# Kernel optimization log

Hardware: AMD Instinct MI355X
Metric: run time of the kernel (lower is better)

Reference implementation:

```python
import jax, jax.numpy as jnp
import numpy as np

N_NODES = 100000
N_EDGES = 1600000
D_IN = 128
D_OUT = 128


def setup_inputs() -> dict:
    key = jax.random.key(0)
    k1, k2, k3, k4 = jax.random.split(key, 4)
    feat = jax.random.normal(k1, (N_NODES, D_IN), dtype=jnp.float32)
    weight = jax.random.normal(k2, (D_IN, D_OUT), dtype=jnp.float32) * (1.0 / np.sqrt(D_IN))
    src = jax.random.randint(k3, (N_EDGES,), 0, N_NODES, dtype=jnp.int64)
    dst = jax.random.randint(k4, (N_EDGES,), 0, N_NODES, dtype=jnp.int64)
    return {"feat": feat, "weight": weight, "src": src, "dst": dst}


def reference(feat, weight, src, dst):
    n = feat.shape[0]
    ones = jnp.ones(src.shape[0], dtype=feat.dtype)
    # norm == 'both': scale source features by out_degree^{-1/2}
    out_deg = jnp.clip(jax.ops.segment_sum(ones, src, num_segments=n), 1.0)
    feat_src = feat * (out_deg ** -0.5)[:, None]  # [N, D_in]
    # update_all(copy_src, sum): gather src features, segment-sum into dst
    agg = jax.ops.segment_sum(feat_src[src], dst, num_segments=n)  # [N, D_in]
    # dense transform with external weight
    rst = agg @ weight  # [N, D_out]
    # destination-side normalization by in_degree^{-1/2}
    in_deg = jnp.clip(jax.ops.segment_sum(ones, dst, num_segments=n), 1.0)
    rst = rst * (in_deg ** -0.5)[:, None]
    return rst
```

## Files before the change

kernel.cpp:

```cpp
#include <hip/hip_runtime.h>
#include <stdint.h>


#define DIM 128
#define BK 64
#define MAXB 2048
#define CAPB 1280
#define SK 128
#define MAXS 1024
#define CAPS 2560
#define PT 512
#define EPT 13
#define CHUNK (PT * EPT)

typedef unsigned int uint;
typedef unsigned short ushortT;
typedef __attribute__((ext_vector_type(8))) _Float16 f16x8;
typedef __attribute__((ext_vector_type(4))) float f32x4;

__device__ __forceinline__ ushortT f2bf(float x) {
    uint u = __float_as_uint(x);
    u = (u + 0x7FFFu + ((u >> 16) & 1u)) >> 16;
    return (ushortT)u;
}
__device__ __forceinline__ float bflo(uint u) { return __uint_as_float(u << 16); }
__device__ __forceinline__ float bfhi(uint u) { return __uint_as_float(u & 0xffff0000u); }

union H16 { _Float16 h; ushortT u; };
__device__ __forceinline__ ushortT f2h_bits(float x) {
    H16 t; t.h = (_Float16)x; return t.u;
}

__global__ __launch_bounds__(PT) void part(
    const int* __restrict__ src, const int* __restrict__ dst,
    int* __restrict__ curB, int* __restrict__ curS,
    int* __restrict__ pairs, unsigned char* __restrict__ srcb,
    int E, int NPB, int NPS) {
    __shared__ int cD[MAXB], lofD[MAXB];
    __shared__ int cS[MAXS], lofS[MAXS];
    __shared__ int bufD[CHUNK];
    __shared__ ushortT bufB[CHUNK];
    __shared__ unsigned char bufS[CHUNK];
    __shared__ int wtotD[8], wtotS[8];

    int tid = threadIdx.x;
    long long base = (long long)blockIdx.x * CHUNK;
    for (int i = tid; i < MAXB; i += PT) cD[i] = 0;
    for (int i = tid; i < MAXS; i += PT) cS[i] = 0;
    __syncthreads();

    int sv[EPT], dv[EPT], lrD[EPT], lrS[EPT];
#pragma unroll
    for (int j = 0; j < EPT; ++j) {
        long long e = base + tid + j * PT;
        bool ok = e < E;
        int s = 0, d = 0;
        if (ok) { s = src[e]; d = dst[e]; }
        sv[j] = s; dv[j] = d;
        lrD[j] = ok ? atomicAdd(&cD[d >> 6], 1) : 0;
        lrS[j] = ok ? atomicAdd(&cS[s >> 7], 1) : 0;
    }
    __syncthreads();

    {
        int lane = tid & 63, wv = tid >> 6;
        int b0 = tid << 2;
        int s0 = cD[b0], s1 = cD[b0 + 1], s2 = cD[b0 + 2], s3 = cD[b0 + 3];
        int tsum = s0 + s1 + s2 + s3;
        int incl = tsum;
        for (int o = 1; o < 64; o <<= 1) {
            int y = __shfl_up(incl, o, 64);
            if (lane >= o) incl += y;
        }
        if (lane == 63) wtotD[wv] = incl;

        int a0idx = tid << 1;
        int t0 = cS[a0idx], t1 = cS[a0idx + 1];
        int ssum = t0 + t1;
        int sincl = ssum;
        for (int o = 1; o < 64; o <<= 1) {
            int y = __shfl_up(sincl, o, 64);
            if (lane >= o) sincl += y;
        }
        if (lane == 63) wtotS[wv] = sincl;
        __syncthreads();

        int wbD = 0, wbS = 0;
        for (int x = 0; x < wv; ++x) { wbD += wtotD[x]; wbS += wtotS[x]; }
        int exD = wbD + incl - tsum;
        lofD[b0] = exD;
        lofD[b0 + 1] = exD + s0;
        lofD[b0 + 2] = exD + s0 + s1;
        lofD[b0 + 3] = exD + s0 + s1 + s2;
        int exS = wbS + sincl - ssum;
        lofS[a0idx] = exS;
        lofS[a0idx + 1] = exS + t0;
    }
    __syncthreads();

    for (int i = tid; i < NPB; i += PT) {
        int c = cD[i];
        cD[i] = c ? atomicAdd(&curB[i], c) : 0;
    }
    for (int i = tid; i < NPS; i += PT) {
        int c = cS[i];
        cS[i] = c ? atomicAdd(&curS[i], c) : 0;
    }

#pragma unroll
    for (int j = 0; j < EPT; ++j) {
        long long e = base + tid + j * PT;
        if (e < E) {
            int b = dv[j] >> 6;
            int pos = lofD[b] + lrD[j];
            bufD[pos] = (sv[j] << 6) | (dv[j] & 63);
            bufB[pos] = (ushortT)b;
            bufS[lofS[sv[j] >> 7] + lrS[j]] = (unsigned char)(sv[j] & 127);
        }
    }
    __syncthreads();

    int cntE = (int)(((long long)E - base < (long long)CHUNK) ? (E - base) : CHUNK);
    for (int i = tid; i < cntE; i += PT) {
        int b = bufB[i];
        int pos = cD[b] + (i - lofD[b]);
        if (pos < CAPB) pairs[(size_t)b * CAPB + pos] = bufD[i];
    }
    for (int i = tid; i < cntE; i += PT) {
        int lo = 0, hi = NPS - 1;
        while (lo < hi) { int mid = (lo + hi + 1) >> 1; if (lofS[mid] <= i) lo = mid; else hi = mid - 1; }
        int pos = cS[lo] + (i - lofS[lo]);
        if (pos < CAPS) srcb[(size_t)lo * CAPS + pos] = bufS[i];
    }
}

__global__ __launch_bounds__(256) void gemm_h(
    const float* __restrict__ feat, const float* __restrict__ W,
    const int* __restrict__ curS, const unsigned char* __restrict__ srcb,
    ushortT* __restrict__ h, int M) {
    __shared__ __align__(16) ushortT Bs[128 * 128];
    __shared__ int hist[SK];

    int tid = threadIdx.x;
    if (tid < SK) hist[tid] = 0;

    {
        int kk = (tid >> 2) << 1;
        int n0 = (tid & 3) << 5;
        const float* w0 = &W[(size_t)kk * DIM + n0];
        const float* w1 = w0 + DIM;
#pragma unroll
        for (int jj = 0; jj < 8; ++jj) {
            float4 a = *(const float4*)&w0[jj * 4];
            float4 b = *(const float4*)&w1[jj * 4];
            float av[4] = {a.x, a.y, a.z, a.w};
            float bv[4] = {b.x, b.y, b.z, b.w};
#pragma unroll
            for (int t = 0; t < 4; ++t) {
                int n = n0 + jj * 4 + t;
                uint u = (uint)f2h_bits(av[t]) | ((uint)f2h_bits(bv[t]) << 16);
                int idx = n * 128 + (((kk >> 3) ^ (n & 7)) << 3) + (kk & 7);
                *(uint*)&Bs[idx] = u;
            }
        }
    }
    __syncthreads();

    int p = blockIdx.x >> 1;
    {
        int cnt = min(curS[p], CAPS);
        const unsigned char* b = &srcb[(size_t)p * CAPS];
        for (int i = tid; i < cnt; i += 256) atomicAdd(&hist[b[i]], 1);
    }
    __syncthreads();

    int wid = tid >> 6;
    int l = tid & 63;
    int lr = l & 15;
    int lk = l >> 4;
    int m0 = blockIdx.x * 64;
    int row = m0 + wid * 16 + lr;
    bool ok = row < M;
    int rr = ok ? row : 0;
    float sc = ok ? rsqrtf((float)max(hist[row & 127], 1)) : 0.f;
    const float* fp = feat + (size_t)rr * DIM;

    f32x4 acc[8];
    f32x4 z = {0.f, 0.f, 0.f, 0.f};
#pragma unroll
    for (int n = 0; n < 8; ++n) acc[n] = z;

#pragma unroll
    for (int kc = 0; kc < 4; ++kc) {
        int kb = kc * 32 + lk * 8;
        float4 x0 = *(const float4*)&fp[kb];
        float4 x1 = *(const float4*)&fp[kb + 4];
        float f[8] = {x0.x * sc, x0.y * sc, x0.z * sc, x0.w * sc,
                      x1.x * sc, x1.y * sc, x1.z * sc, x1.w * sc};
        f16x8 ah, al;
#pragma unroll
        for (int j = 0; j < 8; ++j) {
            _Float16 hi = (_Float16)f[j];
            ah[j] = hi;
            al[j] = (_Float16)(f[j] - (float)hi);
        }
#pragma unroll
        for (int n = 0; n < 8; ++n) {
            int brow = n * 16 + lr;
            int bidx = brow * 128 + (kb ^ ((brow & 7) << 3));
            f16x8 b = *(const f16x8*)&Bs[bidx];
            acc[n] = __builtin_amdgcn_mfma_f32_16x16x32_f16(ah, b, acc[n], 0, 0, 0);
            acc[n] = __builtin_amdgcn_mfma_f32_16x16x32_f16(al, b, acc[n], 0, 0, 0);
        }
    }

#pragma unroll
    for (int r = 0; r < 4; ++r) {
        int ro = m0 + wid * 16 + lk * 4 + r;
        if (ro < M) {
            uint w0 = (uint)f2bf(acc[0][r]) | ((uint)f2bf(acc[1][r]) << 16);
            uint w1 = (uint)f2bf(acc[2][r]) | ((uint)f2bf(acc[3][r]) << 16);
            uint w2 = (uint)f2bf(acc[4][r]) | ((uint)f2bf(acc[5][r]) << 16);
            uint w3 = (uint)f2bf(acc[6][r]) | ((uint)f2bf(acc[7][r]) << 16);
            uint4 o = make_uint4(w0, w1, w2, w3);
            *(uint4*)&h[(size_t)ro * DIM + (lr << 3)] = o;
        }
    }
}

__global__ __launch_bounds__(512) void aggp(
    const ushortT* __restrict__ h, const int* __restrict__ pairs,
    const int* __restrict__ curB, float* __restrict__ out, int N) {
    __shared__ int raw[CAPB];
    __shared__ int sorted[CAPB];
    __shared__ int hist[64], offs[64], cur[64];
    int p = blockIdx.x;
    int tid = threadIdx.x;
    if (tid < 64) hist[tid] = 0;
    __syncthreads();
    int cnt = min(curB[p], CAPB);
    const int* pb = &pairs[(size_t)p * CAPB];
    for (int i = tid; i < cnt; i += 512) {
        int w = pb[i];
        raw[i] = w;
        atomicAdd(&hist[w & 63], 1);
    }
    __syncthreads();
    if (tid < 64) {
        int x = hist[tid], incl = x;
        for (int o = 1; o < 64; o <<= 1) {
            int y = __shfl_up(incl, o, 64);
            if (tid >= o) incl += y;
        }
        offs[tid] = incl - x;
        cur[tid] = incl - x;
    }
    __syncthreads();
    for (int i = tid; i < cnt; i += 512) {
        int w = raw[i];
        int slot = atomicAdd(&cur[w & 63], 1);
        sorted[slot] = w >> 6;
    }
    __syncthreads();
    int g = tid >> 4, c = tid & 15;
    int cb = c << 3;
    for (int nd = g; nd < 64; nd += 32) {
        int node = p * BK + nd;
        if (node >= N) continue;
        int start = offs[nd];
        int degn = hist[nd];
        int end = min(start + degn, CAPB);
        float a0 = 0.f, a1 = 0.f, a2 = 0.f, a3 = 0.f;
        float a4 = 0.f, a5 = 0.f, a6 = 0.f, a7 = 0.f;
        int e = start;
        for (; e + 8 <= end; e += 8) {
            int s0 = sorted[e],     s1 = sorted[e + 1];
            int s2 = sorted[e + 2], s3 = sorted[e + 3];
            int s4 = sorted[e + 4], s5 = sorted[e + 5];
            int s6 = sorted[e + 6], s7 = sorted[e + 7];
            uint4 v0 = *(const uint4*)&h[(size_t)s0 * DIM + cb];
            uint4 v1 = *(const uint4*)&h[(size_t)s1 * DIM + cb];
            uint4 v2 = *(const uint4*)&h[(size_t)s2 * DIM + cb];
            uint4 v3 = *(const uint4*)&h[(size_t)s3 * DIM + cb];
            uint4 v4 = *(const uint4*)&h[(size_t)s4 * DIM + cb];
            uint4 v5 = *(const uint4*)&h[(size_t)s5 * DIM + cb];
            uint4 v6 = *(const uint4*)&h[(size_t)s6 * DIM + cb];
            uint4 v7 = *(const uint4*)&h[(size_t)s7 * DIM + cb];
            a0 += ((bflo(v0.x) + bflo(v1.x)) + (bflo(v2.x) + bflo(v3.x))) +
                  ((bflo(v4.x) + bflo(v5.x)) + (bflo(v6.x) + bflo(v7.x)));
            a1 += ((bfhi(v0.x) + bfhi(v1.x)) + (bfhi(v2.x) + bfhi(v3.x))) +
                  ((bfhi(v4.x) + bfhi(v5.x)) + (bfhi(v6.x) + bfhi(v7.x)));
            a2 += ((bflo(v0.y) + bflo(v1.y)) + (bflo(v2.y) + bflo(v3.y))) +
                  ((bflo(v4.y) + bflo(v5.y)) + (bflo(v6.y) + bflo(v7.y)));
            a3 += ((bfhi(v0.y) + bfhi(v1.y)) + (bfhi(v2.y) + bfhi(v3.y))) +
                  ((bfhi(v4.y) + bfhi(v5.y)) + (bfhi(v6.y) + bfhi(v7.y)));
            a4 += ((bflo(v0.z) + bflo(v1.z)) + (bflo(v2.z) + bflo(v3.z))) +
                  ((bflo(v4.z) + bflo(v5.z)) + (bflo(v6.z) + bflo(v7.z)));
            a5 += ((bfhi(v0.z) + bfhi(v1.z)) + (bfhi(v2.z) + bfhi(v3.z))) +
                  ((bfhi(v4.z) + bfhi(v5.z)) + (bfhi(v6.z) + bfhi(v7.z)));
            a6 += ((bflo(v0.w) + bflo(v1.w)) + (bflo(v2.w) + bflo(v3.w))) +
                  ((bflo(v4.w) + bflo(v5.w)) + (bflo(v6.w) + bflo(v7.w)));
            a7 += ((bfhi(v0.w) + bfhi(v1.w)) + (bfhi(v2.w) + bfhi(v3.w))) +
                  ((bfhi(v4.w) + bfhi(v5.w)) + (bfhi(v6.w) + bfhi(v7.w)));
        }
        for (; e < end; ++e) {
            uint4 v = *(const uint4*)&h[(size_t)sorted[e] * DIM + cb];
            a0 += bflo(v.x); a1 += bfhi(v.x);
            a2 += bflo(v.y); a3 += bfhi(v.y);
            a4 += bflo(v.z); a5 += bfhi(v.z);
            a6 += bflo(v.w); a7 += bfhi(v.w);
        }
        float scn = rsqrtf((float)max(degn, 1));
        size_t ob = (size_t)node * DIM + c;
        out[ob]       = a0 * scn;
        out[ob + 16]  = a1 * scn;
        out[ob + 32]  = a2 * scn;
        out[ob + 48]  = a3 * scn;
        out[ob + 64]  = a4 * scn;
        out[ob + 80]  = a5 * scn;
        out[ob + 96]  = a6 * scn;
        out[ob + 112] = a7 * scn;
    }
}

extern "C" void kernel_launch(void* const* d_in, const int* in_sizes, int n_in,
                              void* d_out, int out_size, void* d_ws, size_t ws_size,
                              hipStream_t stream) {
    const float* feat = (const float*)d_in[0];
    const float* W    = (const float*)d_in[1];
    const int*   src  = (const int*)d_in[2];
    const int*   dst  = (const int*)d_in[3];
    float* out = (float*)d_out;

    int N = in_sizes[0] / DIM;
    int E = in_sizes[2];
    int NPB = (N + BK - 1) / BK;
    int NPS = (N + SK - 1) / SK;

    int* curB = (int*)d_ws;
    int* curS = curB + NPB;
    int* pairs = curS + NPS;
    unsigned char* srcb = (unsigned char*)(pairs + (size_t)NPB * CAPB);
    uintptr_t hp = (uintptr_t)(srcb + (size_t)NPS * CAPS);
    ushortT* h = (ushortT*)((hp + 15) & ~(uintptr_t)15);

    hipMemsetAsync(curB, 0, (size_t)(NPB + NPS) * sizeof(int), stream);

    int nb = (E + CHUNK - 1) / CHUNK;
    part<<<nb, PT, 0, stream>>>(src, dst, curB, curS, pairs, srcb, E, NPB, NPS);
    gemm_h<<<(N + 63) / 64, 256, 0, stream>>>(feat, W, curS, srcb, h, N);
    aggp<<<NPB, 512, 0, stream>>>(h, pairs, curB, out, N);
}
```

Measured before the change: 245.8 us.

## Fuse partition and GEMM into one launch, move source-degree scaling into aggregation

The edge partitioning and the dense feature transform now run as disjoint block ranges of a single kernel, so the GEMM no longer waits for the partition to finish. Because the GEMM runs before source degrees are known, the out-degree scale is taken out of it. A small kernel computes per-node scales, and the aggregation multiplies each gathered row by its source scale. This adds a per-edge scale load and extra multiplies in the gather loop, plus a third launch. The GEMM block also changes to 512 threads with 128 rows per block.

```diff
diff --git a/kernel.cpp b/kernel.cpp
--- a/kernel.cpp
+++ b/kernel.cpp
@@ -31,206 +31,226 @@
     H16 t; t.h = (_Float16)x; return t.u;
 }
 
-__global__ __launch_bounds__(PT) void part(
+#define OFF_CD    0
+#define OFF_LOFD  8192
+#define OFF_CS    16384
+#define OFF_LOFS  20480
+#define OFF_BUFD  24576
+#define OFF_BUFB  51200
+#define OFF_BUFS  64512
+#define OFF_WTOT  71168
+#define SMEM_SZ   71232
+
+__global__ __launch_bounds__(PT) void fusedA(
     const int* __restrict__ src, const int* __restrict__ dst,
     int* __restrict__ curB, int* __restrict__ curS,
     int* __restrict__ pairs, unsigned char* __restrict__ srcb,
-    int E, int NPB, int NPS) {
-    __shared__ int cD[MAXB], lofD[MAXB];
-    __shared__ int cS[MAXS], lofS[MAXS];
-    __shared__ int bufD[CHUNK];
-    __shared__ ushortT bufB[CHUNK];
-    __shared__ unsigned char bufS[CHUNK];
-    __shared__ int wtotD[8], wtotS[8];
-
+    const float* __restrict__ feat, const float* __restrict__ W,
+    ushortT* __restrict__ h,
+    int E, int NPB, int NPS, int M, int NPART) {
+    __shared__ __align__(16) unsigned char smem[SMEM_SZ];
+
+    int bid = blockIdx.x;
     int tid = threadIdx.x;
-    long long base = (long long)blockIdx.x * CHUNK;
-    for (int i = tid; i < MAXB; i += PT) cD[i] = 0;
-    for (int i = tid; i < MAXS; i += PT) cS[i] = 0;
-    __syncthreads();
-
-    int sv[EPT], dv[EPT], lrD[EPT], lrS[EPT];
-#pragma unroll
-    for (int j = 0; j < EPT; ++j) {
-        long long e = base + tid + j * PT;
-        bool ok = e < E;
-        int s = 0, d = 0;
-        if (ok) { s = src[e]; d = dst[e]; }
-        sv[j] = s; dv[j] = d;
-        lrD[j] = ok ? atomicAdd(&cD[d >> 6], 1) : 0;
-        lrS[j] = ok ? atomicAdd(&cS[s >> 7], 1) : 0;
-    }
-    __syncthreads();
-
-    {
-        int lane = tid & 63, wv = tid >> 6;
-        int b0 = tid << 2;
-        int s0 = cD[b0], s1 = cD[b0 + 1], s2 = cD[b0 + 2], s3 = cD[b0 + 3];
-        int tsum = s0 + s1 + s2 + s3;
-        int incl = tsum;
-        for (int o = 1; o < 64; o <<= 1) {
-            int y = __shfl_up(incl, o, 64);
-            if (lane >= o) incl += y;
-        }
-        if (lane == 63) wtotD[wv] = incl;
-
-        int a0idx = tid << 1;
-        int t0 = cS[a0idx], t1 = cS[a0idx + 1];
-        int ssum = t0 + t1;
-        int sincl = ssum;
-        for (int o = 1; o < 64; o <<= 1) {
-            int y = __shfl_up(sincl, o, 64);
-            if (lane >= o) sincl += y;
-        }
-        if (lane == 63) wtotS[wv] = sincl;
-        __syncthreads();
-
-        int wbD = 0, wbS = 0;
-        for (int x = 0; x < wv; ++x) { wbD += wtotD[x]; wbS += wtotS[x]; }
-        int exD = wbD + incl - tsum;
-        lofD[b0] = exD;
-        lofD[b0 + 1] = exD + s0;
-        lofD[b0 + 2] = exD + s0 + s1;
-        lofD[b0 + 3] = exD + s0 + s1 + s2;
-        int exS = wbS + sincl - ssum;
-        lofS[a0idx] = exS;
-        lofS[a0idx + 1] = exS + t0;
-    }
-    __syncthreads();
-
-    for (int i = tid; i < NPB; i += PT) {
-        int c = cD[i];
-        cD[i] = c ? atomicAdd(&curB[i], c) : 0;
-    }
-    for (int i = tid; i < NPS; i += PT) {
-        int c = cS[i];
-        cS[i] = c ? atomicAdd(&curS[i], c) : 0;
-    }
-
-#pragma unroll
-    for (int j = 0; j < EPT; ++j) {
-        long long e = base + tid + j * PT;
-        if (e < E) {
-            int b = dv[j] >> 6;
-            int pos = lofD[b] + lrD[j];
-            bufD[pos] = (sv[j] << 6) | (dv[j] & 63);
-            bufB[pos] = (ushortT)b;
-            bufS[lofS[sv[j] >> 7] + lrS[j]] = (unsigned char)(sv[j] & 127);
-        }
-    }
-    __syncthreads();
-
-    int cntE = (int)(((long long)E - base < (long long)CHUNK) ? (E - base) : CHUNK);
-    for (int i = tid; i < cntE; i += PT) {
-        int b = bufB[i];
-        int pos = cD[b] + (i - lofD[b]);
-        if (pos < CAPB) pairs[(size_t)b * CAPB + pos] = bufD[i];
-    }
-    for (int i = tid; i < cntE; i += PT) {
-        int lo = 0, hi = NPS - 1;
-        while (lo < hi) { int mid = (lo + hi + 1) >> 1; if (lofS[mid] <= i) lo = mid; else hi = mid - 1; }
-        int pos = cS[lo] + (i - lofS[lo]);
-        if (pos < CAPS) srcb[(size_t)lo * CAPS + pos] = bufS[i];
-    }
-}
-
-__global__ __launch_bounds__(256) void gemm_h(
-    const float* __restrict__ feat, const float* __restrict__ W,
+
+    if (bid < NPART) {
+        int* cD = (int*)(smem + OFF_CD);
+        int* lofD = (int*)(smem + OFF_LOFD);
+        int* cS = (int*)(smem + OFF_CS);
+        int* lofS = (int*)(smem + OFF_LOFS);
+        int* bufD = (int*)(smem + OFF_BUFD);
+        ushortT* bufB = (ushortT*)(smem + OFF_BUFB);
+        unsigned char* bufS = (unsigned char*)(smem + OFF_BUFS);
+        int* wtotD = (int*)(smem + OFF_WTOT);
+        int* wtotS = wtotD + 8;
+
+        long long base = (long long)bid * CHUNK;
+        for (int i = tid; i < MAXB; i += PT) cD[i] = 0;
+        for (int i = tid; i < MAXS; i += PT) cS[i] = 0;
+        __syncthreads();
+
+        int sv[EPT], dv[EPT], lrD[EPT], lrS[EPT];
+#pragma unroll
+        for (int j = 0; j < EPT; ++j) {
+            long long e = base + tid + j * PT;
+            bool ok = e < E;
+            int s = 0, d = 0;
+            if (ok) { s = src[e]; d = dst[e]; }
+            sv[j] = s; dv[j] = d;
+            lrD[j] = ok ? atomicAdd(&cD[d >> 6], 1) : 0;
+            lrS[j] = ok ? atomicAdd(&cS[s >> 7], 1) : 0;
+        }
+        __syncthreads();
+
+        {
+            int lane = tid & 63, wv = tid >> 6;
+            int b0 = tid << 2;
+            int s0 = cD[b0], s1 = cD[b0 + 1], s2 = cD[b0 + 2], s3 = cD[b0 + 3];
+            int tsum = s0 + s1 + s2 + s3;
+            int incl = tsum;
+            for (int o = 1; o < 64; o <<= 1) {
+                int y = __shfl_up(incl, o, 64);
+                if (lane >= o) incl += y;
+            }
+            if (lane == 63) wtotD[wv] = incl;
+
+            int a0idx = tid << 1;
+            int t0 = cS[a0idx], t1 = cS[a0idx + 1];
+            int ssum = t0 + t1;
+            int sincl = ssum;
+            for (int o = 1; o < 64; o <<= 1) {
+                int y = __shfl_up(sincl, o, 64);
+                if (lane >= o) sincl += y;
+            }
+            if (lane == 63) wtotS[wv] = sincl;
+            __syncthreads();
+
+            int wbD = 0, wbS = 0;
+            for (int x = 0; x < wv; ++x) { wbD += wtotD[x]; wbS += wtotS[x]; }
+            int exD = wbD + incl - tsum;
+            lofD[b0] = exD;
+            lofD[b0 + 1] = exD + s0;
+            lofD[b0 + 2] = exD + s0 + s1;
+            lofD[b0 + 3] = exD + s0 + s1 + s2;
+            int exS = wbS + sincl - ssum;
+            lofS[a0idx] = exS;
+            lofS[a0idx + 1] = exS + t0;
+        }
+        __syncthreads();
+
+        for (int i = tid; i < NPB; i += PT) {
+            int c = cD[i];
+            cD[i] = c ? atomicAdd(&curB[i], c) : 0;
+        }
+        for (int i = tid; i < NPS; i += PT) {
+            int c = cS[i];
+            cS[i] = c ? atomicAdd(&curS[i], c) : 0;
+        }
+
+#pragma unroll
+        for (int j = 0; j < EPT; ++j) {
+            long long e = base + tid + j * PT;
+            if (e < E) {
+                int b = dv[j] >> 6;
+                int pos = lofD[b] + lrD[j];
+                bufD[pos] = (sv[j] << 6) | (dv[j] & 63);
+                bufB[pos] = (ushortT)b;
+                bufS[lofS[sv[j] >> 7] + lrS[j]] = (unsigned char)(sv[j] & 127);
+            }
+        }
+        __syncthreads();
+
+        int cntE = (int)(((long long)E - base < (long long)CHUNK) ? (E - base) : CHUNK);
+        for (int i = tid; i < cntE; i += PT) {
+            int b = bufB[i];
+            int pos = cD[b] + (i - lofD[b]);
+            if (pos < CAPB) pairs[(size_t)b * CAPB + pos] = bufD[i];
+        }
+        for (int i = tid; i < cntE; i += PT) {
+            int lo = 0, hi = NPS - 1;
+            while (lo < hi) { int mid = (lo + hi + 1) >> 1; if (lofS[mid] <= i) lo = mid; else hi = mid - 1; }
+            int pos = cS[lo] + (i - lofS[lo]);
+            if (pos < CAPS) srcb[(size_t)lo * CAPS + pos] = bufS[i];
+        }
+    } else {
+        ushortT* Bs = (ushortT*)smem;
+
+        {
+            int kk = (tid >> 3) << 1;
+            int n0 = (tid & 7) << 4;
+            const float* w0 = &W[(size_t)kk * DIM + n0];
+            const float* w1 = w0 + DIM;
+#pragma unroll
+            for (int jj = 0; jj < 4; ++jj) {
+                float4 a = *(const float4*)&w0[jj * 4];
+                float4 b = *(const float4*)&w1[jj * 4];
+                float av[4] = {a.x, a.y, a.z, a.w};
+                float bv[4] = {b.x, b.y, b.z, b.w};
+#pragma unroll
+                for (int t = 0; t < 4; ++t) {
+                    int n = n0 + jj * 4 + t;
+                    uint u = (uint)f2h_bits(av[t]) | ((uint)f2h_bits(bv[t]) << 16);
+                    int idx = n * 128 + (((kk >> 3) ^ (n & 7)) << 3) + (kk & 7);
+                    *(uint*)&Bs[idx] = u;
+                }
+            }
+        }
+        __syncthreads();
+
+        int wid = tid >> 6;
+        int l = tid & 63;
+        int lr = l & 15;
+        int lk = l >> 4;
+        int g = bid - NPART;
+        int m0 = g * 128;
+        int row = m0 + wid * 16 + lr;
+        int rr = (row < M) ? row : 0;
+        const float* fp = feat + (size_t)rr * DIM;
+
+        f32x4 acc[8];
+        f32x4 z = {0.f, 0.f, 0.f, 0.f};
+#pragma unroll
+        for (int n = 0; n < 8; ++n) acc[n] = z;
+
+#pragma unroll
+        for (int kc = 0; kc < 4; ++kc) {
+            int kb = kc * 32 + lk * 8;
+            float4 x0 = *(const float4*)&fp[kb];
+            float4 x1 = *(const float4*)&fp[kb + 4];
+            float f[8] = {x0.x, x0.y, x0.z, x0.w, x1.x, x1.y, x1.z, x1.w};
+            f16x8 ah, al;
+#pragma unroll
+            for (int j = 0; j < 8; ++j) {
+                _Float16 hi = (_Float16)f[j];
+                ah[j] = hi;
+                al[j] = (_Float16)(f[j] - (float)hi);
+            }
+#pragma unroll
+            for (int n = 0; n < 8; ++n) {
+                int brow = n * 16 + lr;
+                int bidx = brow * 128 + (kb ^ ((brow & 7) << 3));
+                f16x8 b = *(const f16x8*)&Bs[bidx];
+                acc[n] = __builtin_amdgcn_mfma_f32_16x16x32_f16(ah, b, acc[n], 0, 0, 0);
+                acc[n] = __builtin_amdgcn_mfma_f32_16x16x32_f16(al, b, acc[n], 0, 0, 0);
+            }
+        }
+
+#pragma unroll
+        for (int r = 0; r < 4; ++r) {
+            int ro = m0 + wid * 16 + lk * 4 + r;
+            if (ro < M) {
+                uint w0 = (uint)f2bf(acc[0][r]) | ((uint)f2bf(acc[1][r]) << 16);
+                uint w1 = (uint)f2bf(acc[2][r]) | ((uint)f2bf(acc[3][r]) << 16);
+                uint w2 = (uint)f2bf(acc[4][r]) | ((uint)f2bf(acc[5][r]) << 16);
+                uint w3 = (uint)f2bf(acc[6][r]) | ((uint)f2bf(acc[7][r]) << 16);
+                uint4 o = make_uint4(w0, w1, w2, w3);
+                *(uint4*)&h[(size_t)ro * DIM + (lr << 3)] = o;
+            }
+        }
+    }
+}
+
+__global__ __launch_bounds__(256) void deg(
     const int* __restrict__ curS, const unsigned char* __restrict__ srcb,
-    ushortT* __restrict__ h, int M) {
-    __shared__ __align__(16) ushortT Bs[128 * 128];
+    float* __restrict__ oscale, int N) {
     __shared__ int hist[SK];
-
-    int tid = threadIdx.x;
+    int p = blockIdx.x, tid = threadIdx.x;
     if (tid < SK) hist[tid] = 0;
-
-    {
-        int kk = (tid >> 2) << 1;
-        int n0 = (tid & 3) << 5;
-        const float* w0 = &W[(size_t)kk * DIM + n0];
-        const float* w1 = w0 + DIM;
-#pragma unroll
-        for (int jj = 0; jj < 8; ++jj) {
-            float4 a = *(const float4*)&w0[jj * 4];
-            float4 b = *(const float4*)&w1[jj * 4];
-            float av[4] = {a.x, a.y, a.z, a.w};
-            float bv[4] = {b.x, b.y, b.z, b.w};
-#pragma unroll
-            for (int t = 0; t < 4; ++t) {
-                int n = n0 + jj * 4 + t;
-                uint u = (uint)f2h_bits(av[t]) | ((uint)f2h_bits(bv[t]) << 16);
-                int idx = n * 128 + (((kk >> 3) ^ (n & 7)) << 3) + (kk & 7);
-                *(uint*)&Bs[idx] = u;
-            }
-        }
-    }
-    __syncthreads();
-
-    int p = blockIdx.x >> 1;
-    {
-        int cnt = min(curS[p], CAPS);
-        const unsigned char* b = &srcb[(size_t)p * CAPS];
-        for (int i = tid; i < cnt; i += 256) atomicAdd(&hist[b[i]], 1);
-    }
-    __syncthreads();
-
-    int wid = tid >> 6;
-    int l = tid & 63;
-    int lr = l & 15;
-    int lk = l >> 4;
-    int m0 = blockIdx.x * 64;
-    int row = m0 + wid * 16 + lr;
-    bool ok = row < M;
-    int rr = ok ? row : 0;
-    float sc = ok ? rsqrtf((float)max(hist[row & 127], 1)) : 0.f;
-    const float* fp = feat + (size_t)rr * DIM;
-
-    f32x4 acc[8];
-    f32x4 z = {0.f, 0.f, 0.f, 0.f};
-#pragma unroll
-    for (int n = 0; n < 8; ++n) acc[n] = z;
-
-#pragma unroll
-    for (int kc = 0; kc < 4; ++kc) {
-        int kb = kc * 32 + lk * 8;
-        float4 x0 = *(const float4*)&fp[kb];
-        float4 x1 = *(const float4*)&fp[kb + 4];
-        float f[8] = {x0.x * sc, x0.y * sc, x0.z * sc, x0.w * sc,
-                      x1.x * sc, x1.y * sc, x1.z * sc, x1.w * sc};
-        f16x8 ah, al;
-#pragma unroll
-        for (int j = 0; j < 8; ++j) {
-            _Float16 hi = (_Float16)f[j];
-            ah[j] = hi;
-            al[j] = (_Float16)(f[j] - (float)hi);
-        }
-#pragma unroll
-        for (int n = 0; n < 8; ++n) {
-            int brow = n * 16 + lr;
-            int bidx = brow * 128 + (kb ^ ((brow & 7) << 3));
-            f16x8 b = *(const f16x8*)&Bs[bidx];
-            acc[n] = __builtin_amdgcn_mfma_f32_16x16x32_f16(ah, b, acc[n], 0, 0, 0);
-            acc[n] = __builtin_amdgcn_mfma_f32_16x16x32_f16(al, b, acc[n], 0, 0, 0);
-        }
-    }
-
-#pragma unroll
-    for (int r = 0; r < 4; ++r) {
-        int ro = m0 + wid * 16 + lk * 4 + r;
-        if (ro < M) {
-            uint w0 = (uint)f2bf(acc[0][r]) | ((uint)f2bf(acc[1][r]) << 16);
-            uint w1 = (uint)f2bf(acc[2][r]) | ((uint)f2bf(acc[3][r]) << 16);
-            uint w2 = (uint)f2bf(acc[4][r]) | ((uint)f2bf(acc[5][r]) << 16);
-            uint w3 = (uint)f2bf(acc[6][r]) | ((uint)f2bf(acc[7][r]) << 16);
-            uint4 o = make_uint4(w0, w1, w2, w3);
-            *(uint4*)&h[(size_t)ro * DIM + (lr << 3)] = o;
-        }
+    __syncthreads();
+    int cnt = min(curS[p], CAPS);
+    const unsigned char* b = &srcb[(size_t)p * CAPS];
+    for (int i = tid; i < cnt; i += 256) atomicAdd(&hist[b[i]], 1);
+    __syncthreads();
+    if (tid < SK) {
+        int node = p * SK + tid;
+        if (node < N) oscale[node] = rsqrtf((float)max(hist[tid], 1));
     }
 }
 
 __global__ __launch_bounds__(512) void aggp(
     const ushortT* __restrict__ h, const int* __restrict__ pairs,
-    const int* __restrict__ curB, float* __restrict__ out, int N) {
+    const int* __restrict__ curB, const float* __restrict__ oscale,
+    float* __restrict__ out, int N) {
     __shared__ int raw[CAPB];
     __shared__ int sorted[CAPB];
     __shared__ int hist[64], offs[64], cur[64];
@@ -278,6 +298,8 @@
             int s2 = sorted[e + 2], s3 = sorted[e + 3];
             int s4 = sorted[e + 4], s5 = sorted[e + 5];
             int s6 = sorted[e + 6], s7 = sorted[e + 7];
+            float o0 = oscale[s0], o1 = oscale[s1], o2 = oscale[s2], o3 = oscale[s3];
+            float o4 = oscale[s4], o5 = oscale[s5], o6 = oscale[s6], o7 = oscale[s7];
             uint4 v0 = *(const uint4*)&h[(size_t)s0 * DIM + cb];
             uint4 v1 = *(const uint4*)&h[(size_t)s1 * DIM + cb];
             uint4 v2 = *(const uint4*)&h[(size_t)s2 * DIM + cb];
@@ -286,29 +308,31 @@
             uint4 v5 = *(const uint4*)&h[(size_t)s5 * DIM + cb];
             uint4 v6 = *(const uint4*)&h[(size_t)s6 * DIM + cb];
             uint4 v7 = *(const uint4*)&h[(size_t)s7 * DIM + cb];
-            a0 += ((bflo(v0.x) + bflo(v1.x)) + (bflo(v2.x) + bflo(v3.x))) +
-                  ((bflo(v4.x) + bflo(v5.x)) + (bflo(v6.x) + bflo(v7.x)));
-            a1 += ((bfhi(v0.x) + bfhi(v1.x)) + (bfhi(v2.x) + bfhi(v3.x))) +
-                  ((bfhi(v4.x) + bfhi(v5.x)) + (bfhi(v6.x) + bfhi(v7.x)));
-            a2 += ((bflo(v0.y) + bflo(v1.y)) + (bflo(v2.y) + bflo(v3.y))) +
-                  ((bflo(v4.y) + bflo(v5.y)) + (bflo(v6.y) + bflo(v7.y)));
-            a3 += ((bfhi(v0.y) + bfhi(v1.y)) + (bfhi(v2.y) + bfhi(v3.y))) +
-                  ((bfhi(v4.y) + bfhi(v5.y)) + (bfhi(v6.y) + bfhi(v7.y)));
-            a4 += ((bflo(v0.z) + bflo(v1.z)) + (bflo(v2.z) + bflo(v3.z))) +
-                  ((bflo(v4.z) + bflo(v5.z)) + (bflo(v6.z) + bflo(v7.z)));
-            a5 += ((bfhi(v0.z) + bfhi(v1.z)) + (bfhi(v2.z) + bfhi(v3.z))) +
-                  ((bfhi(v4.z) + bfhi(v5.z)) + (bfhi(v6.z) + bfhi(v7.z)));
-            a6 += ((bflo(v0.w) + bflo(v1.w)) + (bflo(v2.w) + bflo(v3.w))) +
-                  ((bflo(v4.w) + bflo(v5.w)) + (bflo(v6.w) + bflo(v7.w)));
-            a7 += ((bfhi(v0.w) + bfhi(v1.w)) + (bfhi(v2.w) + bfhi(v3.w))) +
-                  ((bfhi(v4.w) + bfhi(v5.w)) + (bfhi(v6.w) + bfhi(v7.w)));
+            a0 += ((o0 * bflo(v0.x) + o1 * bflo(v1.x)) + (o2 * bflo(v2.x) + o3 * bflo(v3.x))) +
+                  ((o4 * bflo(v4.x) + o5 * bflo(v5.x)) + (o6 * bflo(v6.x) + o7 * bflo(v7.x)));
+            a1 += ((o0 * bfhi(v0.x) + o1 * bfhi(v1.x)) + (o2 * bfhi(v2.x) + o3 * bfhi(v3.x))) +
+                  ((o4 * bfhi(v4.x) + o5 * bfhi(v5.x)) + (o6 * bfhi(v6.x) + o7 * bfhi(v7.x)));
+            a2 += ((o0 * bflo(v0.y) + o1 * bflo(v1.y)) + (o2 * bflo(v2.y) + o3 * bflo(v3.y))) +
+                  ((o4 * bflo(v4.y) + o5 * bflo(v5.y)) + (o6 * bflo(v6.y) + o7 * bflo(v7.y)));
+            a3 += ((o0 * bfhi(v0.y) + o1 * bfhi(v1.y)) + (o2 * bfhi(v2.y) + o3 * bfhi(v3.y))) +
+                  ((o4 * bfhi(v4.y) + o5 * bfhi(v5.y)) + (o6 * bfhi(v6.y) + o7 * bfhi(v7.y)));
+            a4 += ((o0 * bflo(v0.z) + o1 * bflo(v1.z)) + (o2 * bflo(v2.z) + o3 * bflo(v3.z))) +
+                  ((o4 * bflo(v4.z) + o5 * bflo(v5.z)) + (o6 * bflo(v6.z) + o7 * bflo(v7.z)));
+            a5 += ((o0 * bfhi(v0.z) + o1 * bfhi(v1.z)) + (o2 * bfhi(v2.z) + o3 * bfhi(v3.z))) +
+                  ((o4 * bfhi(v4.z) + o5 * bfhi(v5.z)) + (o6 * bfhi(v6.z) + o7 * bfhi(v7.z)));
+            a6 += ((o0 * bflo(v0.w) + o1 * bflo(v1.w)) + (o2 * bflo(v2.w) + o3 * bflo(v3.w))) +
+                  ((o4 * bflo(v4.w) + o5 * bflo(v5.w)) + (o6 * bflo(v6.w) + o7 * bflo(v7.w)));
+            a7 += ((o0 * bfhi(v0.w) + o1 * bfhi(v1.w)) + (o2 * bfhi(v2.w) + o3 * bfhi(v3.w))) +
+                  ((o4 * bfhi(v4.w) + o5 * bfhi(v5.w)) + (o6 * bfhi(v6.w) + o7 * bfhi(v7.w)));
         }
         for (; e < end; ++e) {
-            uint4 v = *(const uint4*)&h[(size_t)sorted[e] * DIM + cb];
-            a0 += bflo(v.x); a1 += bfhi(v.x);
-            a2 += bflo(v.y); a3 += bfhi(v.y);
-            a4 += bflo(v.z); a5 += bfhi(v.z);
-            a6 += bflo(v.w); a7 += bfhi(v.w);
+            int se = sorted[e];
+            float os = oscale[se];
+            uint4 v = *(const uint4*)&h[(size_t)se * DIM + cb];
+            a0 += os * bflo(v.x); a1 += os * bfhi(v.x);
+            a2 += os * bflo(v.y); a3 += os * bfhi(v.y);
+            a4 += os * bflo(v.z); a5 += os * bfhi(v.z);
+            a6 += os * bflo(v.w); a7 += os * bfhi(v.w);
         }
         float scn = rsqrtf((float)max(degn, 1));
         size_t ob = (size_t)node * DIM + c;
@@ -339,15 +363,19 @@
 
     int* curB = (int*)d_ws;
     int* curS = curB + NPB;
-    int* pairs = curS + NPS;
+    float* oscale = (float*)(curS + NPS);
+    int* pairs = (int*)(oscale + N);
     unsigned char* srcb = (unsigned char*)(pairs + (size_t)NPB * CAPB);
     uintptr_t hp = (uintptr_t)(srcb + (size_t)NPS * CAPS);
     ushortT* h = (ushortT*)((hp + 15) & ~(uintptr_t)15);
 
     hipMemsetAsync(curB, 0, (size_t)(NPB + NPS) * sizeof(int), stream);
 
-    int nb = (E + CHUNK - 1) / CHUNK;
-    part<<<nb, PT, 0, stream>>>(src, dst, curB, curS, pairs, srcb, E, NPB, NPS);
-    gemm_h<<<(N + 63) / 64, 256, 0, stream>>>(feat, W, curS, srcb, h, N);
-    aggp<<<NPB, 512, 0, stream>>>(h, pairs, curB, out, N);
-}
+    int NPART = (E + CHUNK - 1) / CHUNK;
+    int NGEMM = (N + 127) / 128;
+
+    fusedA<<<NPART + NGEMM, PT, 0, stream>>>(src, dst, curB, curS, pairs, srcb,
+                                             feat, W, h, E, NPB, NPS, N, NPART);
+    deg<<<NPS, 256, 0, stream>>>(curS, srcb, oscale, N);
+    aggp<<<NPB, 512, 0, stream>>>(h, pairs, curB, oscale, out, N);
+}
```

Result: faster. 226.6 us (-7.8%).
